# Performance work log

Hardware: AMD Instinct MI355X
Metric: run time of the kernel (lower is better)

## Reference

```python
import jax, jax.numpy as jnp
import numpy as np

B, T, V = 4, 2048, 32000

def setup_inputs() -> dict:
    key = jax.random.key(0)
    k1, k2 = jax.random.split(key)
    # unnormalized positives -> normalize to a proper categorical distribution per row
    u = jax.random.uniform(k1, (B, T, V), dtype=jnp.float32)
    p = u / jnp.sum(u, axis=-1, keepdims=True)
    # uniform thresholds, one per (batch, time) position (materialized srng draw)
    rng = jax.random.uniform(k2, (B, T), dtype=jnp.float32)
    return {"p": p, "rng": rng}

def reference(p, rng):
    # inverse-CDF categorical sampling:
    # csum[b,t,v] = sum_{w<=v} p[b,t,w]; sample = #{v : rng > csum[v]}
    csum = jnp.cumsum(p, axis=-1)                      # [B, T, V]
    sample = jnp.sum(rng[..., None] > csum, axis=-1)   # [B, T]
    # offset is None in this configuration
    return sample.astype(jnp.int32)
```

## Files before the change

### kernel.cpp

```cpp
#include <hip/hip_runtime.h>


constexpr int V = 32000;
constexpr int FULL_TILES = 31;
constexpr int TAIL_BASE = FULL_TILES * 1024;

__global__ __launch_bounds__(256) void sampler_kernel(
    const float* __restrict__ p,
    const float* __restrict__ rng,
    int* __restrict__ out)
{
    const int row  = blockIdx.x;
    const int tid  = threadIdx.x;
    const int lane = tid & 63;
    const int wave = tid >> 6;

    const float r = rng[row];
    const float4* prow4 = reinterpret_cast<const float4*>(p + (size_t)row * V);

    __shared__ float wsum[4];
    __shared__ int   cpart[4];

    float carry = 0.0f;
    int count = 0;

    for (int tile = 0; tile < FULL_TILES; ++tile) {
        float4 x = prow4[tile * 256 + tid];
        float s = (x.x + x.y) + (x.z + x.w);

        float scan = s;
        #pragma unroll
        for (int off = 1; off < 64; off <<= 1) {
            float n = __shfl_up(scan, off, 64);
            if (lane >= off) scan += n;
        }
        if (lane == 63) wsum[wave] = scan;
        __syncthreads();

        float waveBase = 0.0f, tileTotal = 0.0f;
        #pragma unroll
        for (int w = 0; w < 4; ++w) {
            float t = wsum[w];
            if (w < wave) waveBase += t;
            tileTotal += t;
        }

        float run = carry + waveBase + (scan - s);
        run += x.x; count += (run < r);
        run += x.y; count += (run < r);
        run += x.z; count += (run < r);
        run += x.w; count += (run < r);

        carry += tileTotal;
        __syncthreads();
    }

    {
        float xv = p[(size_t)row * V + TAIL_BASE + tid];
        float scan = xv;
        #pragma unroll
        for (int off = 1; off < 64; off <<= 1) {
            float n = __shfl_up(scan, off, 64);
            if (lane >= off) scan += n;
        }
        if (lane == 63) wsum[wave] = scan;
        __syncthreads();

        float waveBase = 0.0f;
        #pragma unroll
        for (int w = 0; w < 4; ++w) {
            if (w < wave) waveBase += wsum[w];
        }
        float excl = carry + waveBase + (scan - xv);
        count += ((excl + xv) < r);
    }

    #pragma unroll
    for (int off = 32; off > 0; off >>= 1)
        count += __shfl_down(count, off, 64);
    if (lane == 0) cpart[wave] = count;
    __syncthreads();
    if (tid == 0)
        out[row] = cpart[0] + cpart[1] + cpart[2] + cpart[3];
}

extern "C" void kernel_launch(void* const* d_in, const int* in_sizes, int n_in,
                              void* d_out, int out_size, void* d_ws, size_t ws_size,
                              hipStream_t stream) {
    const float* p   = (const float*)d_in[0];
    const float* rng = (const float*)d_in[1];
    int* out = (int*)d_out;
    const int rows = in_sizes[1];
    sampler_kernel<<<rows, 256, 0, stream>>>(p, rng, out);
}
```

Baseline: 1.282 ms.

## Replace tiled block scan with chunk sums and single-chunk search

Each thread now sums a contiguous 128-element chunk. One block-wide scan over the chunk totals then finds the chunk where the CDF crosses the threshold, and only that chunk is re-scanned serially to find the exact index. This removes the 31 per-tile scans and barrier pairs and the final count reduction, at the cost of re-reading one chunk and uncoalesced per-thread strided loads. Float summation order differs from the reference, so counts near the threshold could differ.

```diff
diff --git a/kernel.cpp b/kernel.cpp
--- a/kernel.cpp
+++ b/kernel.cpp
@@ -2,8 +2,8 @@
 
 
 constexpr int V = 32000;
-constexpr int FULL_TILES = 31;
-constexpr int TAIL_BASE = FULL_TILES * 1024;
+constexpr int CHUNK = 128;
+constexpr int NCHUNK = V / CHUNK;
 
 __global__ __launch_bounds__(256) void sampler_kernel(
     const float* __restrict__ p,
@@ -16,72 +16,64 @@
     const int wave = tid >> 6;
 
     const float r = rng[row];
-    const float4* prow4 = reinterpret_cast<const float4*>(p + (size_t)row * V);
+    const float* prow = p + (size_t)row * V;
+    const bool active = (tid < NCHUNK);
 
     __shared__ float wsum[4];
-    __shared__ int   cpart[4];
 
-    float carry = 0.0f;
-    int count = 0;
-
-    for (int tile = 0; tile < FULL_TILES; ++tile) {
-        float4 x = prow4[tile * 256 + tid];
-        float s = (x.x + x.y) + (x.z + x.w);
-
-        float scan = s;
-        #pragma unroll
-        for (int off = 1; off < 64; off <<= 1) {
-            float n = __shfl_up(scan, off, 64);
-            if (lane >= off) scan += n;
+    float S = 0.0f;
+    if (active) {
+        const float4* c4 = reinterpret_cast<const float4*>(prow + tid * CHUNK);
+        float s0 = 0.f, s1 = 0.f, s2 = 0.f, s3 = 0.f;
+        #pragma unroll 2
+        for (int j = 0; j < 32; j += 4) {
+            float4 a = c4[j+0];
+            float4 b = c4[j+1];
+            float4 c = c4[j+2];
+            float4 d = c4[j+3];
+            s0 += (a.x + a.y) + (a.z + a.w);
+            s1 += (b.x + b.y) + (b.z + b.w);
+            s2 += (c.x + c.y) + (c.z + c.w);
+            s3 += (d.x + d.y) + (d.z + d.w);
         }
-        if (lane == 63) wsum[wave] = scan;
-        __syncthreads();
-
-        float waveBase = 0.0f, tileTotal = 0.0f;
-        #pragma unroll
-        for (int w = 0; w < 4; ++w) {
-            float t = wsum[w];
-            if (w < wave) waveBase += t;
-            tileTotal += t;
-        }
-
-        float run = carry + waveBase + (scan - s);
-        run += x.x; count += (run < r);
-        run += x.y; count += (run < r);
-        run += x.z; count += (run < r);
-        run += x.w; count += (run < r);
-
-        carry += tileTotal;
-        __syncthreads();
+        S = (s0 + s1) + (s2 + s3);
     }
 
-    {
-        float xv = p[(size_t)row * V + TAIL_BASE + tid];
-        float scan = xv;
-        #pragma unroll
-        for (int off = 1; off < 64; off <<= 1) {
-            float n = __shfl_up(scan, off, 64);
-            if (lane >= off) scan += n;
+    float scan = S;
+    #pragma unroll
+    for (int off = 1; off < 64; off <<= 1) {
+        float n = __shfl_up(scan, off, 64);
+        if (lane >= off) scan += n;
+    }
+    if (lane == 63) wsum[wave] = scan;
+    __syncthreads();
+
+    float waveBase = 0.0f;
+    #pragma unroll
+    for (int w = 0; w < 4; ++w)
+        if (w < wave) waveBase += wsum[w];
+
+    const float incl = waveBase + scan;
+    float E = __shfl_up(incl, 1, 64);
+    if (lane == 0) E = waveBase;
+
+    if (active && (r <= incl) && (E < r || tid == 0)) {
+        const float4* c4 = reinterpret_cast<const float4*>(prow + tid * CHUNK);
+        float run = E;
+        int cnt = 0;
+        #pragma unroll 4
+        for (int j = 0; j < 32; ++j) {
+            float4 x = c4[j];
+            run += x.x; cnt += (run < r);
+            run += x.y; cnt += (run < r);
+            run += x.z; cnt += (run < r);
+            run += x.w; cnt += (run < r);
         }
-        if (lane == 63) wsum[wave] = scan;
-        __syncthreads();
-
-        float waveBase = 0.0f;
-        #pragma unroll
-        for (int w = 0; w < 4; ++w) {
-            if (w < wave) waveBase += wsum[w];
-        }
-        float excl = carry + waveBase + (scan - xv);
-        count += ((excl + xv) < r);
+        out[row] = tid * CHUNK + cnt;
     }
-
-    #pragma unroll
-    for (int off = 32; off > 0; off >>= 1)
-        count += __shfl_down(count, off, 64);
-    if (lane == 0) cpart[wave] = count;
-    __syncthreads();
-    if (tid == 0)
-        out[row] = cpart[0] + cpart[1] + cpart[2] + cpart[3];
+    if (tid == NCHUNK - 1 && incl < r) {
+        out[row] = V;
+    }
 }
 
 extern "C" void kernel_launch(void* const* d_in, const int* in_sizes, int n_in,
```

Result: no change. 1.285 ms (+0.2%).
